# Optimization experiments

Measured on AMD Instinct MI355X. Metric: run time of the kernel, lower is better.

Reference implementation:

```python
import jax, jax.numpy as jnp
import numpy as np

H_SIZE = 768
N_HEADS = 12
HEAD = H_SIZE // N_HEADS
INTER = 3072
N_LAYERS = 6
VOCAB = 65536
WIDTH = 512  # attention_width
EPS = 1e-6


def rmsnorm(x, w):
    return x * jax.lax.rsqrt(jnp.mean(x * x, axis=-1, keepdims=True) + EPS) * w


def rotate_every_two(x):
    # interleaved rotation: (x0,x1,x2,x3,...) -> (-x1,x0,-x3,x2,...)
    x1 = x[..., ::2]
    x2 = x[..., 1::2]
    return jnp.stack((-x2, x1), axis=-1).reshape(x.shape)


def fixed_pos_embedding(ages, dim):
    # ages: [B,S] float32 -> sin,cos: [B,S,1,dim]
    inv_freq = 1.0 / 10000 ** jnp.linspace(0.0, 2.0, dim // 2)
    t = ages[..., None] * inv_freq  # [B,S,dim//2]
    sin, cos = jnp.sin(t), jnp.cos(t)
    shp = ages.shape + (1, dim)
    sin = jnp.stack((sin, sin), axis=-1).reshape(shp)
    cos = jnp.stack((cos, cos), axis=-1).reshape(shp)
    return sin, cos


def local_attention(q, k, v, width):
    # causal local attention: query i attends to keys j with i-width < j <= i
    B, S, H, D = q.shape
    nb = S // width
    qb = q.reshape(B, nb, width, H, D)
    pad = ((0, 0), (width, 0), (0, 0), (0, 0))
    kp = jnp.pad(k, pad).reshape(B, nb + 1, width, H, D)
    vp = jnp.pad(v, pad).reshape(B, nb + 1, width, H, D)
    k2 = jnp.concatenate((kp[:, :-1], kp[:, 1:]), axis=2)  # [B,nb,2W,H,D]
    v2 = jnp.concatenate((vp[:, :-1], vp[:, 1:]), axis=2)
    scale = 1.0 / jnp.sqrt(jnp.asarray(D, q.dtype))
    scores = jnp.einsum('bnqhd,bnkhd->bnhqk', qb, k2) * scale
    qi = jnp.arange(width)[:, None]
    kj = jnp.arange(2 * width)[None, :]
    blk = jnp.arange(nb)[:, None, None]
    # global: i = b*W+qi, j = b*W - W + kj ; valid: j<=i, i-j<W, j>=0
    valid = (kj > qi) & (kj <= qi + width) & ((blk * width - width + kj) >= 0)
    scores = jnp.where(valid[None, :, None, :, :], scores, -jnp.inf)
    attn = jax.nn.softmax(scores, axis=-1)
    out = jnp.einsum('bnhqk,bnkhd->bnqhd', attn, v2)
    return out.reshape(B, S, H, D)


def encoder_layer(x, sin, cos, p):
    B, S, _ = x.shape
    xn = rmsnorm(x, p['norm_w'])
    qkv = (xn @ p['attn_W'] + p['attn_b']).reshape(B, S, 3, N_HEADS, HEAD)
    q = qkv[:, :, 0] * cos + rotate_every_two(qkv[:, :, 0]) * sin
    k = qkv[:, :, 1] * cos + rotate_every_two(qkv[:, :, 1]) * sin
    v = qkv[:, :, 2]
    attn = local_attention(q, k, v, WIDTH).reshape(B, S, H_SIZE)
    ff = jax.nn.gelu(xn @ p['in_W'] + p['in_b'], approximate=False)
    combined = jnp.concatenate((attn, ff), axis=-1)
    return combined @ p['out_W'] + p['out_b']


def setup_inputs() -> dict:
    key = jax.random.key(0)
    ks = jax.random.split(key, 10)
    B, S = 4, 2048
    std = 0.02
    tokens = jax.random.randint(ks[0], (B, S), 0, VOCAB, dtype=jnp.int64 if jax.config.jax_enable_x64 else jnp.int32)
    ages = jax.random.uniform(ks[1], (B, S), dtype=jnp.float32) * 1000.0
    embed = jax.random.normal(ks[2], (VOCAB, H_SIZE), jnp.float32) * std
    in_norm_w = jnp.ones((H_SIZE,), jnp.float32)
    out_norm_w = jnp.ones((H_SIZE,), jnp.float32)
    norm_w = jnp.ones((N_LAYERS, H_SIZE), jnp.float32)
    attn_W = jax.random.normal(ks[3], (N_LAYERS, H_SIZE, 3 * H_SIZE), jnp.float32) * std
    attn_b = jnp.zeros((N_LAYERS, 3 * H_SIZE), jnp.float32)
    in_W = jax.random.normal(ks[4], (N_LAYERS, H_SIZE, INTER), jnp.float32) * std
    in_b = jnp.zeros((N_LAYERS, INTER), jnp.float32)
    out_W = jax.random.normal(ks[5], (N_LAYERS, H_SIZE + INTER, H_SIZE), jnp.float32) * std
    out_b = jnp.zeros((N_LAYERS, H_SIZE), jnp.float32)
    return {'tokens': tokens, 'ages': ages, 'embed': embed,
            'in_norm_w': in_norm_w, 'out_norm_w': out_norm_w, 'norm_w': norm_w,
            'attn_W': attn_W, 'attn_b': attn_b, 'in_W': in_W, 'in_b': in_b,
            'out_W': out_W, 'out_b': out_b}


def reference(tokens, ages, embed, in_norm_w, out_norm_w, norm_w, attn_W, attn_b, in_W, in_b, out_W, out_b):
    x = embed[tokens]
    x = rmsnorm(x, in_norm_w)
    sin, cos = fixed_pos_embedding(ages, HEAD)
    params = {'norm_w': norm_w, 'attn_W': attn_W, 'attn_b': attn_b,
              'in_W': in_W, 'in_b': in_b, 'out_W': out_W, 'out_b': out_b}

    def step(h, p):
        return h + encoder_layer(h, sin, cos, p), None

    x, _ = jax.lax.scan(step, x, params)
    return rmsnorm(x, out_norm_w)
```

## Files before the change

kernel.cpp:

```cpp
#include <hip/hip_runtime.h>
#include <hip/hip_bf16.h>
#include <math.h>

#define H_SIZE 768
#define N_HEADS 12
#define HEAD 64
#define INTER 3072
#define N_LAYERS 6
#define BATCH 4
#define SEQ 2048
#define BS (BATCH*SEQ)
#define EPSV 1e-6f

typedef __attribute__((ext_vector_type(8))) short bf16x8;
typedef __attribute__((ext_vector_type(4))) float f32x4;
typedef unsigned short u16;

__device__ inline float bf2f(u16 v) {
    union { float f; unsigned u; } x; x.u = ((unsigned)v) << 16; return x.f;
}
__device__ inline u16 f2bf(float f) {
    union { float f; unsigned u; } x; x.f = f;
    unsigned u = x.u;
    return (u16)((u + 0x7FFFu + ((u >> 16) & 1u)) >> 16);
}

__device__ __forceinline__ void stage16(const u16* g, u16* ldsbase) {
    __builtin_amdgcn_global_load_lds((const __attribute__((address_space(1))) void*)g,
                                     (__attribute__((address_space(3))) void*)ldsbase,
                                     16, 0, 0);
}

__device__ __forceinline__ size_t apk_idx(int mf, int KB, int kb, int lane) {
    return ((size_t)mf * KB + kb) * 512 + lane * 8;
}

__global__ void probe_kernel(const u16* __restrict__ embed, const int* __restrict__ tokens,
                             int* __restrict__ flags) {
    if (threadIdx.x == 0 && blockIdx.x == 0) {
        int good = 0, evenzero = 0;
        for (int i = 0; i < 128; i++) {
            u16 h = embed[i];
            int e = (h >> 7) & 0xFF;
            if (h == 0 || (e >= 87 && e <= 133)) good++;
            if ((i & 1) == 0 && h == 0) evenzero++;
        }
        flags[0] = (evenzero >= 48) ? 1 : ((good >= 110) ? 0 : 1);
        int z = 0;
        for (int i = 0; i < 64; i++) if (tokens[2 * i + 1] == 0) z++;
        flags[1] = (z >= 60) ? 1 : 0;
    }
}

__global__ __launch_bounds__(256) void sincos_kernel(const void* __restrict__ ages,
                                                     float* __restrict__ SIN,
                                                     float* __restrict__ COS,
                                                     const int* __restrict__ flags) {
    int idx = blockIdx.x * 256 + threadIdx.x;
    if (idx >= BS * 32) return;
    bool f32in = flags[0] != 0;
    int row = idx >> 5, f = idx & 31;
    float age = f32in ? ((const float*)ages)[row] : bf2f(((const u16*)ages)[row]);
    float inv = expf(-(2.0f * (float)f / 31.0f) * 9.210340371976184f);
    float t = age * inv;
    SIN[idx] = sinf(t);
    COS[idx] = cosf(t);
}

__global__ __launch_bounds__(256) void wtrans_kernel(const void* __restrict__ Wsrc,
                                                     u16* __restrict__ Wt,
                                                     int K, int N, size_t ltstride,
                                                     const int* __restrict__ flags) {
    __shared__ u16 tile[64][72];
    bool f32in = flags[0] != 0;
    int l = blockIdx.z;
    const float* W32 = (const float*)Wsrc + (size_t)l * K * N;
    const u16*   W16 = (const u16*)Wsrc + (size_t)l * K * N;
    u16* out = Wt + (size_t)l * ltstride;
    int k0 = blockIdx.y * 64, n0 = blockIdx.x * 64;
    int t = threadIdx.x;
    int kk = t >> 3, nn = (t & 7) * 8;
#pragma unroll
    for (int it = 0; it < 2; it++) {
        int kr = kk + it * 32;
        u16 tmp[8];
        if (f32in) {
            const float* src = W32 + (size_t)(k0 + kr) * N + n0 + nn;
            float4 f0 = *(const float4*)src, f1 = *(const float4*)(src + 4);
            tmp[0] = f2bf(f0.x); tmp[1] = f2bf(f0.y); tmp[2] = f2bf(f0.z); tmp[3] = f2bf(f0.w);
            tmp[4] = f2bf(f1.x); tmp[5] = f2bf(f1.y); tmp[6] = f2bf(f1.z); tmp[7] = f2bf(f1.w);
        } else {
            uint4 v = *(const uint4*)(W16 + (size_t)(k0 + kr) * N + n0 + nn);
            const u16* pv = (const u16*)&v;
#pragma unroll
            for (int i = 0; i < 8; i++) tmp[i] = pv[i];
        }
        *(uint4*)(&tile[kr][nn]) = *(const uint4*)tmp;
    }
    __syncthreads();
    int n = t >> 3, kq = (t & 7) * 8;
#pragma unroll
    for (int it = 0; it < 2; it++) {
        int nr = n + it * 32;
        u16 tmp[8];
#pragma unroll
        for (int i = 0; i < 8; i++) tmp[i] = tile[kq + i][nr];
        *(uint4*)(out + (size_t)(n0 + nr) * K + k0 + kq) = *(const uint4*)tmp;
    }
}

__global__ __launch_bounds__(256) void bias_conv_kernel(const void* __restrict__ ab,
                                                        const void* __restrict__ ib,
                                                        const void* __restrict__ ob,
                                                        u16* __restrict__ dst,
                                                        const int* __restrict__ flags) {
    int i = blockIdx.x * 256 + threadIdx.x;
    bool f32in = flags[0] != 0;
    const int A = 6 * 2304, B = 6 * 3072, C = 6 * 768;
    if (i < A) dst[i] = f32in ? f2bf(((const float*)ab)[i]) : ((const u16*)ab)[i];
    else if (i < A + B) { int j = i - A; dst[i] = f32in ? f2bf(((const float*)ib)[j]) : ((const u16*)ib)[j]; }
    else if (i < A + B + C) { int j = i - A - B; dst[i] = f32in ? f2bf(((const float*)ob)[j]) : ((const u16*)ob)[j]; }
}

__global__ __launch_bounds__(256) void embed_norm_kernel(const int* __restrict__ tokens,
                                                         const void* __restrict__ embed,
                                                         const void* __restrict__ wbase,
                                                         float* __restrict__ X,
                                                         const int* __restrict__ flags) {
    int row = blockIdx.x * 4 + (threadIdx.x >> 6);
    int lane = threadIdx.x & 63;
    bool f32in = flags[0] != 0;
    bool i64 = flags[1] != 0;
    int tok = i64 ? tokens[2 * row] : tokens[row];
    tok &= 65535;
    const u16* er16 = (const u16*)embed + (size_t)tok * H_SIZE;
    const float* er32 = (const float*)embed + (size_t)tok * H_SIZE;
    const u16* w16 = (const u16*)wbase;
    const float* w32 = (const float*)wbase;
    float v[12]; float ss = 0.f;
#pragma unroll
    for (int k = 0; k < 12; k++) {
        int i = lane + k * 64;
        float t = f32in ? er32[i] : bf2f(er16[i]);
        v[k] = t; ss += t * t;
    }
#pragma unroll
    for (int off = 1; off < 64; off <<= 1) ss += __shfl_xor(ss, off, 64);
    float scale = rsqrtf(ss * (1.0f / 768.0f) + EPSV);
#pragma unroll
    for (int k = 0; k < 12; k++) {
        int i = lane + k * 64;
        float wv = f32in ? w32[i] : bf2f(w16[i]);
        X[(size_t)row * H_SIZE + i] = v[k] * scale * wv;
    }
}

__global__ __launch_bounds__(256) void rmsnorm_kernel(const float* __restrict__ X,
                                                      const void* __restrict__ wbase, size_t woff,
                                                      void* __restrict__ Y,
                                                      const int* __restrict__ flags) {
    int row = blockIdx.x * 4 + (threadIdx.x >> 6);
    int lane = threadIdx.x & 63;
    bool f32in = flags[0] != 0;
    const u16* w16 = (const u16*)wbase + woff;
    const float* w32 = (const float*)wbase + woff;
    const float* xr = X + (size_t)row * H_SIZE;
    float v[12]; float ss = 0.f;
#pragma unroll
    for (int k = 0; k < 12; k++) { v[k] = xr[lane + k * 64]; ss += v[k] * v[k]; }
#pragma unroll
    for (int off = 1; off < 64; off <<= 1) ss += __shfl_xor(ss, off, 64);
    float scale = rsqrtf(ss * (1.0f / 768.0f) + EPSV);
#pragma unroll
    for (int k = 0; k < 12; k++) {
        int i = lane + k * 64;
        float wv = f32in ? w32[i] : bf2f(w16[i]);
        float val = v[k] * scale * wv;
        if (f32in) ((float*)Y)[(size_t)row * H_SIZE + i] = val;
        else       ((u16*)Y)[(size_t)row * H_SIZE + i] = f2bf(val);
    }
}

__global__ __launch_bounds__(256) void rmsnorm_pack_kernel(const float* __restrict__ X,
                                                           const void* __restrict__ wbase, size_t woff,
                                                           u16* __restrict__ Apk,
                                                           const int* __restrict__ flags) {
    __shared__ u16 tile[16][776];
    int lane = threadIdx.x & 63, wave = threadIdx.x >> 6;
    bool f32in = flags[0] != 0;
    const u16* w16 = (const u16*)wbase + woff;
    const float* w32 = (const float*)wbase + woff;
    int blk = blockIdx.x;
#pragma unroll
    for (int rep = 0; rep < 4; rep++) {
        int r16 = rep * 4 + wave;
        const float* xr = X + (size_t)(blk * 16 + r16) * H_SIZE;
        float v[12]; float ss = 0.f;
#pragma unroll
        for (int k = 0; k < 12; k++) { v[k] = xr[lane + k * 64]; ss += v[k] * v[k]; }
#pragma unroll
        for (int off = 1; off < 64; off <<= 1) ss += __shfl_xor(ss, off, 64);
        float scale = rsqrtf(ss * (1.0f / 768.0f) + EPSV);
#pragma unroll
        for (int k = 0; k < 12; k++) {
            int i = lane + k * 64;
            float wv = f32in ? w32[i] : bf2f(w16[i]);
            tile[r16][i] = f2bf(v[k] * scale * wv);
        }
    }
    __syncthreads();
#pragma unroll
    for (int it = 0; it < 6; it++) {
        int idx = it * 256 + threadIdx.x;
        int kb = idx >> 6, l2 = idx & 63;
        int g2 = l2 >> 4, r16 = l2 & 15;
        uint4 v = *(const uint4*)(&tile[r16][kb * 32 + g2 * 8]);
        *(uint4*)(Apk + apk_idx(blk, 24, kb, l2)) = v;
    }
}

template <int EPI, int BN, int MGRP>
__global__ __launch_bounds__(256) void gemm_kernel(const u16* __restrict__ Apk,
                                                   const u16* __restrict__ Wt,
                                                   const u16* __restrict__ abias,
                                                   const u16* __restrict__ bbias,
                                                   float* __restrict__ Cf,
                                                   u16* __restrict__ qkvb,
                                                   u16* __restrict__ combpk,
                                                   int K,
                                                   const float* __restrict__ SIN,
                                                   const float* __restrict__ COS) {
    constexpr int NF = BN / 32;
    constexpr int VCS = (BN == 128) ? 6 : 5;
    __shared__ u16 Bl[3][BN][32];
    const int tid = threadIdx.x;
    const int lane = tid & 63, wave = tid >> 6;
    const int wm = wave >> 1, wn = wave & 1;
    const int lm = lane & 15, g = lane >> 4;
    const int KB = K >> 5;

    const int nx = gridDim.x;
    const int mpx = gridDim.y >> 3;
    int linear = blockIdx.y * nx + blockIdx.x;
    const int xcd = linear & 7;
    int wch = linear >> 3;
    const int grpsz = MGRP * nx;
    int grp = wch / grpsz;
    int rem = wch - grp * grpsz;
    int n_idx = rem / MGRP;
    int m_loc = grp * MGRP + (rem - n_idx * MGRP);
    const int m0 = (xcd * mpx + m_loc) * 128;
    const int n0 = n_idx * BN;
    const int mf0 = (m0 >> 4) + wm * 4;

    f32x4 acc[4][NF];
#pragma unroll
    for (int i = 0; i < 4; i++)
#pragma unroll
        for (int j = 0; j < NF; j++) acc[i][j] = (f32x4)0.0f;

    const int swcol = ((lane & 3) ^ ((lane >> 3) & 3)) * 8;
    const u16* gb = Wt + (size_t)(n0 + wave * 16 + (lane >> 2)) * K + swcol;
    const size_t row64 = (size_t)64 * K;

    bf16x8 afA[4], afB[4];

#define LOAD_A(AF, T) do {                                                        \
        _Pragma("unroll")                                                         \
        for (int i_ = 0; i_ < 4; i_++)                                            \
            AF[i_] = *(const bf16x8*)(Apk + apk_idx(mf0 + i_, KB, (T) >> 5, lane)); \
    } while (0)

#define STAGE_B(BI, KK) do {                                          \
        stage16(gb + (KK), &Bl[BI][wave * 16][0]);                    \
        if (BN == 128) stage16(gb + row64 + (KK), &Bl[BI][64 + wave * 16][0]); \
    } while (0)

    const int cc = (g ^ ((lm >> 1) & 3)) * 8;

#define GBODY(BUF, NXT, AFC, AFN, T) do {                                         \
        if ((T) + 32 < K) { asm volatile("s_waitcnt vmcnt(%0)" :: "i"(VCS) : "memory"); } \
        else              { asm volatile("s_waitcnt vmcnt(4)" ::: "memory"); }    \
        __builtin_amdgcn_s_barrier();                                             \
        if ((T) + 32 < K) LOAD_A(AFN, (T) + 32);                                  \
        if ((T) + 64 < K) STAGE_B(NXT, (T) + 64);                                 \
        bf16x8 b[NF];                                                             \
        _Pragma("unroll")                                                         \
        for (int j_ = 0; j_ < NF; j_++)                                           \
            b[j_] = *(const bf16x8*)(&Bl[BUF][wn * (BN / 2) + j_ * 16 + lm][cc]); \
        __builtin_amdgcn_s_setprio(1);                                            \
        _Pragma("unroll")                                                         \
        for (int i_ = 0; i_ < 4; i_++)                                            \
            _Pragma("unroll")                                                     \
            for (int j_ = 0; j_ < NF; j_++)                                       \
                acc[i_][j_] = __builtin_amdgcn_mfma_f32_16x16x32_bf16(AFC[i_], b[j_], acc[i_][j_], 0, 0, 0); \
        __builtin_amdgcn_s_setprio(0);                                            \
    } while (0)

    STAGE_B(0, 0);
    STAGE_B(1, 32);
    LOAD_A(afA, 0);

    for (int k0 = 0; k0 < K; k0 += 192) {
        GBODY(0, 2, afA, afB, k0);
        GBODY(1, 0, afB, afA, k0 + 32);
        GBODY(2, 1, afA, afB, k0 + 64);
        GBODY(0, 2, afB, afA, k0 + 96);
        GBODY(1, 0, afA, afB, k0 + 128);
        GBODY(2, 1, afB, afA, k0 + 160);
    }

#undef GBODY
#undef STAGE_B
#undef LOAD_A

#pragma unroll
    for (int i = 0; i < 4; i++) {
        int mbase = m0 + wm * 64 + i * 16 + g * 4;
#pragma unroll
        for (int j = 0; j < NF; j++) {
            int n = n0 + wn * (BN / 2) + j * 16 + lm;
            float bv;
            if (EPI == 0) bv = (n < 2304) ? bf2f(abias[n]) : bf2f(bbias[n - 2304]);
            else          bv = bf2f(abias[n]);
#pragma unroll
            for (int r = 0; r < 4; r++) {
                float v = acc[i][j][r] + bv;
                int mm = mbase + r;
                if (EPI == 0) {
                    float p = __shfl_xor(v, 1);
                    if (n < 2304) {
                        float outv = v;
                        if (n < 1536) {
                            int f = (n >> 1) & 31;
                            float c = COS[mm * 32 + f], s = SIN[mm * 32 + f];
                            outv = (n & 1) ? (v * c + p * s) : (v * c - p * s);
                        }
                        qkvb[(size_t)mm * 2304 + n] = f2bf(outv);
                    } else {
                        float u = 0.7978845608f * (v + 0.044715f * v * v * v);
                        float e = __expf(2.0f * u);
                        float th = 1.0f - 2.0f / (e + 1.0f);
                        int k = n - 1536;
                        int lp = ((k >> 3) & 3) * 16 + (mm & 15);
                        combpk[apk_idx(mm >> 4, 120, k >> 5, lp) + (k & 7)] = f2bf(0.5f * v * (1.0f + th));
                    }
                } else {
                    Cf[(size_t)mm * 768 + n] += v;
                }
            }
        }
    }
}

__global__ __launch_bounds__(512) void attn_kernel(const u16* __restrict__ qkv,
                                                   u16* __restrict__ combpk) {
    __shared__ u16 Qs[128][72];
    __shared__ u16 Ks[64][72];
    __shared__ u16 Vt[64][72];
    __shared__ u16 Ps[8][16][72];

    const int tid = threadIdx.x;
    const int lane = tid & 63, wave = tid >> 6;
    const int lm = lane & 15, g = lane >> 4;
    const int q0 = blockIdx.x * 128;
    const int h = blockIdx.y;
    const int b = blockIdx.z;
    const size_t rowbase = (size_t)b * SEQ;

#pragma unroll
    for (int it = 0; it < 2; ++it) {
        int idx = tid + it * 512;
        int r = idx >> 3, u = (idx & 7) * 8;
        uint4 v = *(const uint4*)(qkv + (rowbase + q0 + r) * 2304 + h * HEAD + u);
        *(uint4*)(&Qs[r][u]) = v;
    }

    float m_r[4], l_r[4];
    f32x4 o[4];
#pragma unroll
    for (int r = 0; r < 4; r++) { m_r[r] = -INFINITY; l_r[r] = 0.f; }
#pragma unroll
    for (int d = 0; d < 4; d++) o[d] = (f32x4)0.0f;

    const int c_start = (q0 < 512) ? ((512 - q0) >> 6) : 0;
    for (int c = c_start; c < 10; ++c) {
        int kc = q0 - 512 + c * 64;
        __syncthreads();
        {
            int r = tid >> 3, u = (tid & 7) * 8;
            int j = kc + r;
            uint4 kv = make_uint4(0, 0, 0, 0), vv = make_uint4(0, 0, 0, 0);
            if (j >= 0) {
                kv = *(const uint4*)(qkv + (rowbase + j) * 2304 + 768 + h * HEAD + u);
                vv = *(const uint4*)(qkv + (rowbase + j) * 2304 + 1536 + h * HEAD + u);
            }
            *(uint4*)(&Ks[r][u]) = kv;
            const u16* pv = (const u16*)&vv;
#pragma unroll
            for (int i = 0; i < 8; i++) Vt[u + i][r] = pv[i];
        }
        __syncthreads();

        bf16x8 aq0 = *(const bf16x8*)(&Qs[wave * 16 + lm][g * 8]);
        bf16x8 aq1 = *(const bf16x8*)(&Qs[wave * 16 + lm][32 + g * 8]);
        f32x4 s[4];
#pragma unroll
        for (int kf = 0; kf < 4; kf++) {
            bf16x8 b0 = *(const bf16x8*)(&Ks[kf * 16 + lm][g * 8]);
            bf16x8 b1 = *(const bf16x8*)(&Ks[kf * 16 + lm][32 + g * 8]);
            f32x4 z = (f32x4)0.0f;
            z = __builtin_amdgcn_mfma_f32_16x16x32_bf16(aq0, b0, z, 0, 0, 0);
            z = __builtin_amdgcn_mfma_f32_16x16x32_bf16(aq1, b1, z, 0, 0, 0);
            s[kf] = z;
        }

        float sv[4][4], mc[4];
#pragma unroll
        for (int r = 0; r < 4; r++) mc[r] = -INFINITY;
#pragma unroll
        for (int kf = 0; kf < 4; kf++) {
            int j = kc + kf * 16 + lm;
#pragma unroll
            for (int r = 0; r < 4; r++) {
                int i = q0 + wave * 16 + g * 4 + r;
                bool valid = (j >= 0) && (j <= i) && (j >= i - 511);
                float v = valid ? s[kf][r] * 0.125f : -INFINITY;
                sv[kf][r] = v;
                mc[r] = fmaxf(mc[r], v);
            }
        }
#pragma unroll
        for (int off = 1; off < 16; off <<= 1)
#pragma unroll
            for (int r = 0; r < 4; r++) mc[r] = fmaxf(mc[r], __shfl_xor(mc[r], off, 64));

        float alpha[4], mn[4];
#pragma unroll
        for (int r = 0; r < 4; r++) {
            mn[r] = fmaxf(m_r[r], mc[r]);
            alpha[r] = (mn[r] > -1e37f) ? __expf(m_r[r] - mn[r]) : 1.0f;
            m_r[r] = mn[r];
        }
        float ps[4][4], rs[4] = {0.f, 0.f, 0.f, 0.f};
#pragma unroll
        for (int kf = 0; kf < 4; kf++)
#pragma unroll
            for (int r = 0; r < 4; r++) {
                float p = (sv[kf][r] > -1e37f) ? __expf(sv[kf][r] - mn[r]) : 0.0f;
                ps[kf][r] = p;
                rs[r] += p;
            }
#pragma unroll
        for (int off = 1; off < 16; off <<= 1)
#pragma unroll
            for (int r = 0; r < 4; r++) rs[r] += __shfl_xor(rs[r], off, 64);
#pragma unroll
        for (int r = 0; r < 4; r++) l_r[r] = l_r[r] * alpha[r] + rs[r];

#pragma unroll
        for (int kf = 0; kf < 4; kf++)
#pragma unroll
            for (int r = 0; r < 4; r++) Ps[wave][g * 4 + r][kf * 16 + lm] = f2bf(ps[kf][r]);

#pragma unroll
        for (int d = 0; d < 4; d++)
#pragma unroll
            for (int r = 0; r < 4; r++) o[d][r] *= alpha[r];

        bf16x8 pa0 = *(const bf16x8*)(&Ps[wave][lm][g * 8]);
        bf16x8 pa1 = *(const bf16x8*)(&Ps[wave][lm][32 + g * 8]);
#pragma unroll
        for (int d = 0; d < 4; d++) {
            bf16x8 b0 = *(const bf16x8*)(&Vt[d * 16 + lm][g * 8]);
            bf16x8 b1 = *(const bf16x8*)(&Vt[d * 16 + lm][32 + g * 8]);
            o[d] = __builtin_amdgcn_mfma_f32_16x16x32_bf16(pa0, b0, o[d], 0, 0, 0);
            o[d] = __builtin_amdgcn_mfma_f32_16x16x32_bf16(pa1, b1, o[d], 0, 0, 0);
        }
    }

#pragma unroll
    for (int d = 0; d < 4; d++) {
        int dd = d * 16 + lm;
        int k = h * HEAD + dd;
        int kb = k >> 5;
        int gsub = (k >> 3) & 3;
#pragma unroll
        for (int r = 0; r < 4; r++) {
            int R = (int)rowbase + q0 + wave * 16 + g * 4 + r;
            float v = o[d][r] / l_r[r];
            int lp = gsub * 16 + (R & 15);
            combpk[apk_idx(R >> 4, 120, kb, lp) + (k & 7)] = f2bf(v);
        }
    }
}

extern "C" void kernel_launch(void* const* d_in, const int* in_sizes, int n_in,
                              void* d_out, int out_size, void* d_ws, size_t ws_size,
                              hipStream_t stream) {
    const int* tokens   = (const int*)d_in[0];
    const void* ages    = d_in[1];
    const void* embed   = d_in[2];
    const void* in_norm_w  = d_in[3];
    const void* out_norm_w = d_in[4];
    const void* norm_w     = d_in[5];
    const void* attn_W     = d_in[6];
    const void* attn_b     = d_in[7];
    const void* in_W       = d_in[8];
    const void* in_b       = d_in[9];
    const void* out_W      = d_in[10];
    const void* out_b      = d_in[11];

    char* w = (char*)d_ws;
    int* flags  = (int*)w;   w += 256;
    float* x    = (float*)w; w += (size_t)BS * H_SIZE * 4;
    u16* xnpk   = (u16*)w;   w += (size_t)(BS / 16) * 24 * 1024;
    u16* qkv    = (u16*)w;   w += (size_t)BS * 2304 * 2;
    u16* combpk = (u16*)w;   w += (size_t)(BS / 16) * 120 * 1024;
    float* sinb = (float*)w; w += (size_t)BS * 32 * 4;
    float* cosb = (float*)w; w += (size_t)BS * 32 * 4;
    u16* wtf    = (u16*)w;   w += (size_t)N_LAYERS * 5376 * 768 * 2;
    u16* wto    = (u16*)w;   w += (size_t)N_LAYERS * 768 * 3840 * 2;
    u16* biasb  = (u16*)w;   w += (size_t)(6*2304 + 6*3072 + 6*768) * 2;

    u16* ab_b = biasb;
    u16* ib_b = biasb + 6 * 2304;
    u16* ob_b = ib_b + 6 * 3072;

    const size_t LFS = (size_t)5376 * 768;

    probe_kernel<<<1, 64, 0, stream>>>((const u16*)embed, tokens, flags);
    sincos_kernel<<<(BS * 32 + 255) / 256, 256, 0, stream>>>(ages, sinb, cosb, flags);
    embed_norm_kernel<<<BS / 4, 256, 0, stream>>>(tokens, embed, in_norm_w, x, flags);
    bias_conv_kernel<<<(6 * (2304 + 3072 + 768) + 255) / 256, 256, 0, stream>>>(
        attn_b, in_b, out_b, biasb, flags);

    wtrans_kernel<<<dim3(2304 / 64, 768 / 64, N_LAYERS), 256, 0, stream>>>(
        attn_W, wtf, 768, 2304, LFS, flags);
    wtrans_kernel<<<dim3(3072 / 64, 768 / 64, N_LAYERS), 256, 0, stream>>>(
        in_W, wtf + (size_t)2304 * 768, 768, 3072, LFS, flags);
    wtrans_kernel<<<dim3(768 / 64, 3840 / 64, N_LAYERS), 256, 0, stream>>>(
        out_W, wto, 3840, 768, (size_t)768 * 3840, flags);

    for (int l = 0; l < N_LAYERS; ++l) {
        rmsnorm_pack_kernel<<<BS / 16, 256, 0, stream>>>(x, norm_w, (size_t)l * H_SIZE, xnpk, flags);
        gemm_kernel<0, 128, 8><<<dim3(5376 / 128, BS / 128), 256, 0, stream>>>(
            xnpk, wtf + (size_t)l * LFS, ab_b + l * 2304, ib_b + l * 3072,
            nullptr, qkv, combpk, H_SIZE, sinb, cosb);
        attn_kernel<<<dim3(SEQ / 128, N_HEADS, BATCH), 512, 0, stream>>>(qkv, combpk);
        gemm_kernel<2, 64, 2><<<dim3(768 / 64, BS / 128), 256, 0, stream>>>(
            combpk, wto + (size_t)l * 768 * 3840, ob_b + l * 768, nullptr,
            x, nullptr, nullptr, H_SIZE + INTER, nullptr, nullptr);
    }
    rmsnorm_kernel<<<BS / 4, 256, 0, stream>>>(x, out_norm_w, 0, d_out, flags);
}
```

Baseline: 1.903 ms.

## Prepack weights into MFMA fragment layout and load B directly to registers

The weight transpose kernel now writes B in the same fragment-packed layout as A, so each lane can load its bf16x8 B fragment straight from global memory. The GEMM drops the LDS-staged B path, its barriers and swizzle, and instead keeps a three-deep register pipeline of A and B fragments, waiting on vmcnt. This removes LDS traffic and workgroup barriers but duplicates B loads across the two wm waves and raises register pressure and global/L2 bandwidth demand.

Result: no change. 1.882 ms (-1.1%).

```diff
diff --git a/kernel.cpp b/kernel.cpp
--- a/kernel.cpp
+++ b/kernel.cpp
@@ -25,14 +25,8 @@
     return (u16)((u + 0x7FFFu + ((u >> 16) & 1u)) >> 16);
 }
 
-__device__ __forceinline__ void stage16(const u16* g, u16* ldsbase) {
-    __builtin_amdgcn_global_load_lds((const __attribute__((address_space(1))) void*)g,
-                                     (__attribute__((address_space(3))) void*)ldsbase,
-                                     16, 0, 0);
-}
-
-__device__ __forceinline__ size_t apk_idx(int mf, int KB, int kb, int lane) {
-    return ((size_t)mf * KB + kb) * 512 + lane * 8;
+__device__ __forceinline__ size_t apk_idx(int f, int KB, int kb, int lane) {
+    return ((size_t)f * KB + kb) * 512 + lane * 8;
 }
 
 __global__ void probe_kernel(const u16* __restrict__ embed, const int* __restrict__ tokens,
@@ -68,7 +62,7 @@
 }
 
 __global__ __launch_bounds__(256) void wtrans_kernel(const void* __restrict__ Wsrc,
-                                                     u16* __restrict__ Wt,
+                                                     u16* __restrict__ Bpk,
                                                      int K, int N, size_t ltstride,
                                                      const int* __restrict__ flags) {
     __shared__ u16 tile[64][72];
@@ -76,10 +70,11 @@
     int l = blockIdx.z;
     const float* W32 = (const float*)Wsrc + (size_t)l * K * N;
     const u16*   W16 = (const u16*)Wsrc + (size_t)l * K * N;
-    u16* out = Wt + (size_t)l * ltstride;
+    u16* out = Bpk + (size_t)l * ltstride;
     int k0 = blockIdx.y * 64, n0 = blockIdx.x * 64;
     int t = threadIdx.x;
     int kk = t >> 3, nn = (t & 7) * 8;
+    const int KB = K >> 5;
 #pragma unroll
     for (int it = 0; it < 2; it++) {
         int kr = kk + it * 32;
@@ -98,14 +93,18 @@
         *(uint4*)(&tile[kr][nn]) = *(const uint4*)tmp;
     }
     __syncthreads();
-    int n = t >> 3, kq = (t & 7) * 8;
 #pragma unroll
     for (int it = 0; it < 2; it++) {
-        int nr = n + it * 32;
+        int idx = it * 256 + t;
+        int nr = idx >> 3;
+        int kq8 = idx & 7;
         u16 tmp[8];
 #pragma unroll
-        for (int i = 0; i < 8; i++) tmp[i] = tile[kq + i][nr];
-        *(uint4*)(out + (size_t)(n0 + nr) * K + k0 + kq) = *(const uint4*)tmp;
+        for (int i = 0; i < 8; i++) tmp[i] = tile[kq8 * 8 + i][nr];
+        int nf = (n0 + nr) >> 4;
+        int kb = (k0 >> 5) + (kq8 >> 2);
+        int lp = (kq8 & 3) * 16 + (nr & 15);
+        *(uint4*)(out + apk_idx(nf, KB, kb, lp)) = *(const uint4*)tmp;
     }
 }
 
@@ -221,7 +220,7 @@
 
 template <int EPI, int BN, int MGRP>
 __global__ __launch_bounds__(256) void gemm_kernel(const u16* __restrict__ Apk,
-                                                   const u16* __restrict__ Wt,
+                                                   const u16* __restrict__ Bpk,
                                                    const u16* __restrict__ abias,
                                                    const u16* __restrict__ bbias,
                                                    float* __restrict__ Cf,
@@ -231,8 +230,7 @@
                                                    const float* __restrict__ SIN,
                                                    const float* __restrict__ COS) {
     constexpr int NF = BN / 32;
-    constexpr int VCS = (BN == 128) ? 6 : 5;
-    __shared__ u16 Bl[3][BN][32];
+    constexpr int LPB = 4 + NF;
     const int tid = threadIdx.x;
     const int lane = tid & 63, wave = tid >> 6;
     const int wm = wave >> 1, wn = wave & 1;
@@ -252,6 +250,7 @@
     const int m0 = (xcd * mpx + m_loc) * 128;
     const int n0 = n_idx * BN;
     const int mf0 = (m0 >> 4) + wm * 4;
+    const int nf0 = (n0 >> 4) + wn * (BN >> 5);
 
     f32x4 acc[4][NF];
 #pragma unroll
@@ -259,60 +258,41 @@
 #pragma unroll
         for (int j = 0; j < NF; j++) acc[i][j] = (f32x4)0.0f;
 
-    const int swcol = ((lane & 3) ^ ((lane >> 3) & 3)) * 8;
-    const u16* gb = Wt + (size_t)(n0 + wave * 16 + (lane >> 2)) * K + swcol;
-    const size_t row64 = (size_t)64 * K;
-
-    bf16x8 afA[4], afB[4];
-
-#define LOAD_A(AF, T) do {                                                        \
-        _Pragma("unroll")                                                         \
-        for (int i_ = 0; i_ < 4; i_++)                                            \
-            AF[i_] = *(const bf16x8*)(Apk + apk_idx(mf0 + i_, KB, (T) >> 5, lane)); \
+    bf16x8 a0[4], a1[4], a2[4];
+    bf16x8 b0[NF], b1[NF], b2[NF];
+
+#define LOADSET(AS, BS_, KBI) do {                                                  \
+        _Pragma("unroll")                                                           \
+        for (int i_ = 0; i_ < 4; i_++)                                              \
+            AS[i_] = *(const bf16x8*)(Apk + apk_idx(mf0 + i_, KB, (KBI), lane));    \
+        _Pragma("unroll")                                                           \
+        for (int j_ = 0; j_ < NF; j_++)                                             \
+            BS_[j_] = *(const bf16x8*)(Bpk + apk_idx(nf0 + j_, KB, (KBI), lane));   \
     } while (0)
 
-#define STAGE_B(BI, KK) do {                                          \
-        stage16(gb + (KK), &Bl[BI][wave * 16][0]);                    \
-        if (BN == 128) stage16(gb + row64 + (KK), &Bl[BI][64 + wave * 16][0]); \
+#define GBODY(AS, BS_, AN, BN_, T) do {                                             \
+        if ((T) + 1 < KB) { asm volatile("s_waitcnt vmcnt(%0)" :: "i"(LPB) : "memory"); } \
+        else              { asm volatile("s_waitcnt vmcnt(0)" ::: "memory"); }      \
+        if ((T) + 2 < KB) LOADSET(AN, BN_, (T) + 2);                                \
+        __builtin_amdgcn_s_setprio(1);                                              \
+        _Pragma("unroll")                                                           \
+        for (int i_ = 0; i_ < 4; i_++)                                              \
+            _Pragma("unroll")                                                       \
+            for (int j_ = 0; j_ < NF; j_++)                                         \
+                acc[i_][j_] = __builtin_amdgcn_mfma_f32_16x16x32_bf16(AS[i_], BS_[j_], acc[i_][j_], 0, 0, 0); \
+        __builtin_amdgcn_s_setprio(0);                                              \
     } while (0)
 
-    const int cc = (g ^ ((lm >> 1) & 3)) * 8;
-
-#define GBODY(BUF, NXT, AFC, AFN, T) do {                                         \
-        if ((T) + 32 < K) { asm volatile("s_waitcnt vmcnt(%0)" :: "i"(VCS) : "memory"); } \
-        else              { asm volatile("s_waitcnt vmcnt(4)" ::: "memory"); }    \
-        __builtin_amdgcn_s_barrier();                                             \
-        if ((T) + 32 < K) LOAD_A(AFN, (T) + 32);                                  \
-        if ((T) + 64 < K) STAGE_B(NXT, (T) + 64);                                 \
-        bf16x8 b[NF];                                                             \
-        _Pragma("unroll")                                                         \
-        for (int j_ = 0; j_ < NF; j_++)                                           \
-            b[j_] = *(const bf16x8*)(&Bl[BUF][wn * (BN / 2) + j_ * 16 + lm][cc]); \
-        __builtin_amdgcn_s_setprio(1);                                            \
-        _Pragma("unroll")                                                         \
-        for (int i_ = 0; i_ < 4; i_++)                                            \
-            _Pragma("unroll")                                                     \
-            for (int j_ = 0; j_ < NF; j_++)                                       \
-                acc[i_][j_] = __builtin_amdgcn_mfma_f32_16x16x32_bf16(AFC[i_], b[j_], acc[i_][j_], 0, 0, 0); \
-        __builtin_amdgcn_s_setprio(0);                                            \
-    } while (0)
-
-    STAGE_B(0, 0);
-    STAGE_B(1, 32);
-    LOAD_A(afA, 0);
-
-    for (int k0 = 0; k0 < K; k0 += 192) {
-        GBODY(0, 2, afA, afB, k0);
-        GBODY(1, 0, afB, afA, k0 + 32);
-        GBODY(2, 1, afA, afB, k0 + 64);
-        GBODY(0, 2, afB, afA, k0 + 96);
-        GBODY(1, 0, afA, afB, k0 + 128);
-        GBODY(2, 1, afB, afA, k0 + 160);
+    LOADSET(a0, b0, 0);
+    LOADSET(a1, b1, 1);
+    for (int t = 0; t < KB; t += 3) {
+        GBODY(a0, b0, a2, b2, t);
+        GBODY(a1, b1, a0, b0, t + 1);
+        GBODY(a2, b2, a1, b1, t + 2);
     }
 
 #undef GBODY
-#undef STAGE_B
-#undef LOAD_A
+#undef LOADSET
 
 #pragma unroll
     for (int i = 0; i < 4; i++) {
```
